# Kernel optimization log

Hardware: AMD Instinct MI355X
Metric: run time of the kernel (lower is better)

The kernel has to match this reference:

```python
import jax, jax.numpy as jnp
import numpy as np
import math

STRIDE = ((2, 2), (4, 4), (8, 8), (16, 16))  # (ws, hs) pairs
D_MODEL = 256
B, H, W = 8, 128, 128
BN_EPS = 1e-5
LEAKY_SLOPE = 0.2


def setup_inputs() -> dict:
    key = jax.random.key(0)
    ks = jax.random.split(key, 8)
    s = 1.0 / math.sqrt(D_MODEL)
    s3 = 1.0 / math.sqrt(D_MODEL * 9)
    return {
        "x": jax.random.normal(ks[0], (B, D_MODEL, H, W), jnp.float32),
        "wq": jax.random.normal(ks[1], (D_MODEL, D_MODEL, 1, 1), jnp.float32) * s,
        "bq": jnp.zeros((D_MODEL,), jnp.float32),
        "wk": jax.random.normal(ks[2], (D_MODEL, D_MODEL, 1, 1), jnp.float32) * s,
        "bk": jnp.zeros((D_MODEL,), jnp.float32),
        "wv": jax.random.normal(ks[3], (D_MODEL, D_MODEL, 1, 1), jnp.float32) * s,
        "bv": jnp.zeros((D_MODEL,), jnp.float32),
        "wo": jax.random.normal(ks[4], (D_MODEL, D_MODEL, 3, 3), jnp.float32) * s3,
        "bo": jnp.zeros((D_MODEL,), jnp.float32),
        "gamma": jnp.ones((D_MODEL,), jnp.float32),
        "beta": jnp.zeros((D_MODEL,), jnp.float32),
    }


def _conv1x1(x, w, bias):
    # 1x1 conv == channel matmul
    return jnp.einsum('bchw,oc->bohw', x, w[:, :, 0, 0]) + bias[None, :, None, None]


def reference(x, wq, bq, wk, bk, wv, bv, wo, bo, gamma, beta):
    b, c, h, w = x.shape
    n = len(STRIDE)
    d_k = c // n
    q = _conv1x1(x, wq, bq)
    k = _conv1x1(x, wk, bk)
    v = _conv1x1(x, wv, bv)
    outs = []
    for idx, (ws, hs) in enumerate(STRIDE):
        lo = idx * d_k
        oh, ow = h // hs, w // ws

        def gather(t):
            # strided patch gather: element (i,j) head <- t[:, :, i::hs, j::ws]
            t = t[:, lo:lo + d_k].reshape(b, d_k, oh, hs, ow, ws)
            return t.transpose(0, 3, 5, 1, 2, 4).reshape(b, hs * ws, d_k * oh * ow)

        qi, ki, vi = gather(q), gather(k), gather(v)
        scale = 1.0 / jnp.sqrt(jnp.asarray(qi.shape[-1], qi.dtype))
        scores = jnp.einsum('bsd,btd->bst', qi, ki) * scale  # [b, hs*ws, hs*ws]
        p = jax.nn.softmax(scores, axis=-1)
        y = jnp.einsum('bst,btd->bsd', p, vi)
        # scatter back exactly as the torch permute(0,3,1,4,2,5): h = i*oh + row
        y = y.reshape(b, hs, ws, d_k, oh, ow).transpose(0, 3, 1, 4, 2, 5).reshape(b, d_k, h, w)
        outs.append(y)
    out = jnp.concatenate(outs, axis=1)  # [b, c, h, w]
    # output_linear: 3x3 conv -> BatchNorm2d (training-mode batch stats) -> LeakyReLU(0.2)
    out = jax.lax.conv_general_dilated(out, wo, (1, 1), 'SAME',
                                       dimension_numbers=('NCHW', 'OIHW', 'NCHW'))
    out = out + bo[None, :, None, None]
    mean = out.mean(axis=(0, 2, 3))
    var = out.var(axis=(0, 2, 3))
    out = (out - mean[None, :, None, None]) * jax.lax.rsqrt(var[None, :, None, None] + BN_EPS)
    out = out * gamma[None, :, None, None] + beta[None, :, None, None]
    return jnp.where(out > 0, out, LEAKY_SLOPE * out)
```

## Files before the change

### kernel.cpp

```cpp
#include <hip/hip_runtime.h>
#include <stdint.h>


#define DEVI static __device__ __forceinline__

typedef short bf8 __attribute__((ext_vector_type(8)));
typedef float f32x4 __attribute__((ext_vector_type(4)));

DEVI unsigned short f2bf(float f) {
  unsigned u = __builtin_bit_cast(unsigned, f);
  u = (u + 0x7fffu + ((u >> 16) & 1u)) >> 16;
  return (unsigned short)u;
}
DEVI float bf2f(unsigned short h) {
  unsigned u = ((unsigned)h) << 16;
  return __builtin_bit_cast(float, u);
}

DEVI void gload16(const void* g, void* l) {
  __builtin_amdgcn_global_load_lds(
      (const __attribute__((address_space(1))) unsigned int*)g,
      (__attribute__((address_space(3))) unsigned int*)l, 16, 0, 0);
}

static const size_t WB_OFF  = 0;
static const size_t WOB_OFF = 393216;
static const size_t QN_OFF  = 1572864;
static const size_t KN_OFF  = QN_OFF + 67108864;
static const size_t VN_OFF  = KN_OFF + 67108864;
static const size_t YN_OFF  = VN_OFF + 67108864;
static const size_t SC_OFF  = YN_OFF + 67108864;
static const size_t PRB_OFF = SC_OFF + 2236928;
static const size_t BNP_OFF = PRB_OFF + 1118464;
static const size_t BNS_OFF = BNP_OFF + 4194304;
static const size_t ZP_OFF  = BNS_OFF + 2048;
static const size_t WS_NEED = ZP_OFF + 256;

__global__ void k_prep(const float* __restrict__ wq, const float* __restrict__ wk,
                       const float* __restrict__ wv, const float* __restrict__ wo,
                       unsigned short* __restrict__ Wb, unsigned short* __restrict__ Wob) {
  int i = blockIdx.x * 256 + threadIdx.x;
  if (i < 196608) {
    int z = i >> 16, r = i & 65535;
    const float* w = (z == 0) ? wq : (z == 1) ? wk : wv;
    Wb[i] = f2bf(w[r]);
  } else {
    int j = i - 196608;
    int o = j / 2304, k = j - o * 2304;
    int e = k >> 8, c = k & 255;
    Wob[j] = f2bf(wo[(o * 256 + c) * 9 + e]);
  }
}

__global__ void k_zero(float* __restrict__ p, int n) {
  int i = blockIdx.x * 256 + threadIdx.x;
  for (; i < n; i += gridDim.x * 256) p[i] = 0.f;
}

__global__ __launch_bounds__(256) void k_qkv(
    const float* __restrict__ x, const unsigned short* __restrict__ Wb,
    const float* __restrict__ bq, const float* __restrict__ bk, const float* __restrict__ bv,
    unsigned short* __restrict__ Qn, unsigned short* __restrict__ Kn,
    unsigned short* __restrict__ Vn) {
  const int pt = blockIdx.x, b = blockIdx.y;
  const int p0 = pt * 64;
  const int tid = threadIdx.x;

  __shared__ __align__(16) unsigned short xt[64 * 256];
  __shared__ __align__(16) unsigned short ot[64 * 256];

  const float* xb = x + (size_t)b * 256 * 16384;
  for (int k = 0; k < 16; ++k) {
    int i = tid + k * 256;
    int c = i >> 4, p4 = (i & 15) * 4;
    float4 v = *(const float4*)(xb + (size_t)c * 16384 + p0 + p4);
    xt[(p4 + 0) * 256 + (c ^ (((p4 + 0) & 7) << 3))] = f2bf(v.x);
    xt[(p4 + 1) * 256 + (c ^ (((p4 + 1) & 7) << 3))] = f2bf(v.y);
    xt[(p4 + 2) * 256 + (c ^ (((p4 + 2) & 7) << 3))] = f2bf(v.z);
    xt[(p4 + 3) * 256 + (c ^ (((p4 + 3) & 7) << 3))] = f2bf(v.w);
  }
  __syncthreads();

  const int wave = tid >> 6, lane = tid & 63;
  const int lr = lane & 15, lk = lane >> 4;
  const int obase = wave * 64;

  for (int z = 0; z < 3; ++z) {
    const unsigned short* Wz = Wb + (size_t)z * 65536;
    f32x4 acc[4][4];
    for (int m = 0; m < 4; ++m)
      for (int n = 0; n < 4; ++n)
        for (int r = 0; r < 4; ++r) acc[m][n][r] = 0.f;

    for (int ks = 0; ks < 8; ++ks) {
      int c0 = ks * 32 + lk * 8;
      bf8 a[4], bb[4];
#pragma unroll
      for (int m = 0; m < 4; ++m)
        a[m] = *(const bf8*)(Wz + (size_t)(obase + m * 16 + lr) * 256 + c0);
#pragma unroll
      for (int n = 0; n < 4; ++n) {
        int p = n * 16 + lr;
        bb[n] = *(const bf8*)(&xt[p * 256 + (c0 ^ ((p & 7) << 3))]);
      }
#pragma unroll
      for (int m = 0; m < 4; ++m)
#pragma unroll
        for (int n = 0; n < 4; ++n)
          acc[m][n] = __builtin_amdgcn_mfma_f32_16x16x32_bf16(a[m], bb[n], acc[m][n], 0, 0, 0);
    }

    const float* bias = (z == 0) ? bq : (z == 1) ? bk : bv;
    unsigned short* On = (z == 0) ? Qn : (z == 1) ? Kn : Vn;
    __syncthreads();
#pragma unroll
    for (int m = 0; m < 4; ++m) {
      int ob4 = obase + m * 16 + lk * 4;
      float4 b4 = *(const float4*)(bias + ob4);
#pragma unroll
      for (int n = 0; n < 4; ++n) {
        int p = n * 16 + lr;
        ushort4 v4;
        v4.x = f2bf(acc[m][n][0] + b4.x);
        v4.y = f2bf(acc[m][n][1] + b4.y);
        v4.z = f2bf(acc[m][n][2] + b4.z);
        v4.w = f2bf(acc[m][n][3] + b4.w);
        *(ushort4*)(&ot[p * 256 + (ob4 ^ ((p & 7) << 3))]) = v4;
      }
    }
    __syncthreads();
    unsigned short* gb = On + ((size_t)b * 16384 + p0) * 256;
#pragma unroll
    for (int i = 0; i < 8; ++i) {
      int ch = tid + i * 256;
      *(uint4*)(gb + ch * 8) = *(const uint4*)(&ot[ch * 8]);
    }
  }
}

template <int IDX>
__global__ __launch_bounds__(256) void k_gram(
    const unsigned short* __restrict__ Qn, const unsigned short* __restrict__ Kn,
    float* __restrict__ scores) {
  constexpr int HS = 2 << IDX, S = HS * HS, OH = 64 >> IDX, NSP = OH * OH;
  constexpr int SPW = (IDX == 2) ? 2 : 8;
  constexpr int DSUB = SPW * 64;
  constexpr int SPB = NSP / 32;
  constexpr int STEPS = SPB / SPW;
  constexpr int ROWS = S;
  constexpr int TPT = S * SPW * 8 / 256;
  constexpr int SCOFF = (IDX == 0) ? 0 : (IDX == 1) ? 128 : 2176;
  constexpr int HC = IDX * 64;
  constexpr int MT = (IDX == 2) ? 4 : 1;

  const int chk = blockIdx.x, b = blockIdx.y;
  const int tid = threadIdx.x;
  const int wave = tid >> 6, lane = tid & 63, lr = lane & 15, lk = lane >> 4;

  __shared__ __align__(16) unsigned short qg[ROWS * DSUB];
  __shared__ __align__(16) unsigned short kg[ROWS * DSUB];
  __shared__ float red[S * S];

  const size_t base = (size_t)b * 16384 * 256;

  f32x4 acc[MT][MT];
  for (int m = 0; m < MT; ++m)
    for (int n = 0; n < MT; ++n)
      for (int r = 0; r < 4; ++r) acc[m][n][r] = 0.f;

  for (int st = 0; st < STEPS; ++st) {
    const int sp0 = chk * SPB + st * SPW;
    __syncthreads();
#pragma unroll
    for (int r = 0; r < TPT; ++r) {
      int task = tid + r * 256;
      int cg = task & 7, pl = task >> 3;
      int spl = pl >> (2 * (IDX + 1)), s = pl & (S - 1);
      int sp = sp0 + spl;
      int ohi = sp >> (6 - IDX), owi = sp & (OH - 1);
      int ii = s >> (IDX + 1), jj = s & (HS - 1);
      int p = (ohi * HS + ii) * 128 + owi * HS + jj;
      size_t gaddr = base + (size_t)p * 256 + HC + ((cg ^ (p & 7)) << 3);
      int laddr = s * DSUB + (((spl * 8 + cg) ^ (s & 7)) << 3);
      *(uint4*)(qg + laddr) = *(const uint4*)(Qn + gaddr);
      *(uint4*)(kg + laddr) = *(const uint4*)(Kn + gaddr);
    }
    __syncthreads();
    if (IDX == 2) {
      int kgid = wave * 4 + lk;
      bf8 a[4], bb[4];
#pragma unroll
      for (int m = 0; m < 4; ++m) {
        int row = m * 16 + lr;
        int off = row * DSUB + ((kgid ^ (row & 7)) << 3);
        a[m] = *(const bf8*)(qg + off);
        bb[m] = *(const bf8*)(kg + off);
      }
#pragma unroll
      for (int m = 0; m < 4; ++m)
#pragma unroll
        for (int n = 0; n < 4; ++n)
          acc[m][n] = __builtin_amdgcn_mfma_f32_16x16x32_bf16(a[m], bb[n], acc[m][n], 0, 0, 0);
    } else {
      int row = lr & (ROWS - 1);
#pragma unroll
      for (int kk = 0; kk < 4; ++kk) {
        int kgid = (wave * 4 + kk) * 4 + lk;
        int off = row * DSUB + ((kgid ^ (row & 7)) << 3);
        bf8 a = *(const bf8*)(qg + off);
        bf8 bb = *(const bf8*)(kg + off);
        acc[0][0] = __builtin_amdgcn_mfma_f32_16x16x32_bf16(a, bb, acc[0][0], 0, 0, 0);
      }
    }
  }

  __syncthreads();
  for (int i2 = tid; i2 < S * S; i2 += 256) red[i2] = 0.f;
  __syncthreads();
  if (IDX == 2) {
#pragma unroll
    for (int m = 0; m < 4; ++m)
#pragma unroll
      for (int n = 0; n < 4; ++n)
#pragma unroll
        for (int r = 0; r < 4; ++r)
          atomicAdd(&red[(m * 16 + lk * 4 + r) * 64 + n * 16 + lr], acc[m][n][r]);
  } else if (IDX == 1) {
#pragma unroll
    for (int r = 0; r < 4; ++r)
      atomicAdd(&red[(lk * 4 + r) * 16 + lr], acc[0][0][r]);
  } else {
    if (lk == 0 && lr < 4) {
#pragma unroll
      for (int r = 0; r < 4; ++r)
        atomicAdd(&red[r * 4 + lr], acc[0][0][r]);
    }
  }
  __syncthreads();
  float* sc = scores + SCOFF + (size_t)b * S * S;
  for (int i2 = tid; i2 < S * S; i2 += 256) atomicAdd(sc + i2, red[i2]);
}

__global__ __launch_bounds__(256) void k_gram3(
    const unsigned short* __restrict__ Qn, const unsigned short* __restrict__ Kn,
    float* __restrict__ part3) {
  const int qc = blockIdx.x, tq = blockIdx.y, b = blockIdx.z;
  const int tid = threadIdx.x;
  const int wave = tid >> 6, lane = tid & 63, lr = lane & 15, lk = lane >> 4;

  __shared__ __align__(16) unsigned short qg[256 * 64];
  __shared__ __align__(16) unsigned short kg[64 * 64];

  const size_t base = (size_t)b * 16384 * 256;

  f32x4 acc[4][4];
  for (int m = 0; m < 4; ++m)
    for (int n = 0; n < 4; ++n)
      for (int r = 0; r < 4; ++r) acc[m][n][r] = 0.f;

  for (int st = 0; st < 8; ++st) {
    int sp = qc * 8 + st;
    int ohi = sp >> 3, owi = sp & 7;
    __syncthreads();
#pragma unroll
    for (int r = 0; r < 8; ++r) {
      int task = tid + r * 256;
      int cg = task & 7, s = task >> 3;
      int p = (ohi * 16 + (s >> 4)) * 128 + owi * 16 + (s & 15);
      uint4 v = *(const uint4*)(Qn + base + (size_t)p * 256 + 192 + ((cg ^ (p & 7)) << 3));
      *(uint4*)(qg + s * 64 + ((cg ^ (s & 7)) << 3)) = v;
    }
#pragma unroll
    for (int r = 0; r < 2; ++r) {
      int task = tid + r * 256;
      int cg = task & 7, tl = task >> 3;
      int p = (ohi * 16 + tq * 4 + (tl >> 4)) * 128 + owi * 16 + (tl & 15);
      uint4 v = *(const uint4*)(Kn + base + (size_t)p * 256 + 192 + ((cg ^ (p & 7)) << 3));
      *(uint4*)(kg + tl * 64 + ((cg ^ (tl & 7)) << 3)) = v;
    }
    __syncthreads();
#pragma unroll
    for (int kk = 0; kk < 2; ++kk) {
      int kgid = kk * 4 + lk;
      bf8 a[4], bb[4];
#pragma unroll
      for (int m = 0; m < 4; ++m) {
        int row = wave * 64 + m * 16 + lr;
        a[m] = *(const bf8*)(qg + row * 64 + ((kgid ^ (row & 7)) << 3));
      }
#pragma unroll
      for (int n = 0; n < 4; ++n) {
        int rowb = n * 16 + lr;
        bb[n] = *(const bf8*)(kg + rowb * 64 + ((kgid ^ (rowb & 7)) << 3));
      }
#pragma unroll
      for (int m = 0; m < 4; ++m)
#pragma unroll
        for (int n = 0; n < 4; ++n)
          acc[m][n] = __builtin_amdgcn_mfma_f32_16x16x32_bf16(a[m], bb[n], acc[m][n], 0, 0, 0);
    }
  }

  float* pb = part3 + (((size_t)qc * 8 + b) * 65536);
#pragma unroll
  for (int m = 0; m < 4; ++m)
#pragma unroll
    for (int r = 0; r < 4; ++r) {
      int srow = wave * 64 + m * 16 + lk * 4 + r;
#pragma unroll
      for (int n = 0; n < 4; ++n)
        pb[srow * 256 + tq * 64 + n * 16 + lr] = acc[m][n][r];
    }
}

__global__ __launch_bounds__(256) void k_softmax(const float* __restrict__ scores,
                                                 unsigned short* __restrict__ prb) {
  const int idx = blockIdx.x, b = blockIdx.y;
  const int S = 4 << (2 * idx);
  const int off = (idx == 0 ? 0 : idx == 1 ? 128 : 2176) + b * S * S;
  const int s = threadIdx.x;
  if (s >= S) return;
  const float scale = rsqrtf(64.0f * (float)(4096 >> (2 * idx)));
  const float* row = scores + off + s * S;
  float m = -1e30f;
  for (int t = 0; t < S; ++t) m = fmaxf(m, row[t]);
  m *= scale;
  float sum = 0.f;
  for (int t = 0; t < S; ++t) sum += __expf(row[t] * scale - m);
  float inv = 1.0f / sum;
  unsigned short* prow = prb + off + s * S;
  for (int t = 0; t < S; ++t) prow[t] = f2bf(__expf(row[t] * scale - m) * inv);
}

__global__ __launch_bounds__(256) void k_softmax3(const float* __restrict__ part3,
                                                  unsigned short* __restrict__ prb) {
  const int sc_ = blockIdx.x, b = blockIdx.y;
  const int tid = threadIdx.x;
  const int s = sc_ * 32 + (tid >> 3);
  const int t0 = (tid & 7) * 32;
  float v[32];
#pragma unroll
  for (int k = 0; k < 32; ++k) v[k] = 0.f;
  for (int q = 0; q < 8; ++q) {
    const float4* pp = (const float4*)(part3 + (((size_t)q * 8 + b) * 256 + s) * 256 + t0);
#pragma unroll
    for (int k = 0; k < 8; ++k) {
      float4 u = pp[k];
      v[k * 4 + 0] += u.x; v[k * 4 + 1] += u.y; v[k * 4 + 2] += u.z; v[k * 4 + 3] += u.w;
    }
  }
  const float scale = 1.0f / 64.0f;
  float m = -1e30f;
#pragma unroll
  for (int k = 0; k < 32; ++k) { v[k] *= scale; m = fmaxf(m, v[k]); }
  m = fmaxf(m, __shfl_xor(m, 1));
  m = fmaxf(m, __shfl_xor(m, 2));
  m = fmaxf(m, __shfl_xor(m, 4));
  float sum = 0.f;
#pragma unroll
  for (int k = 0; k < 32; ++k) { v[k] = __expf(v[k] - m); sum += v[k]; }
  sum += __shfl_xor(sum, 1);
  sum += __shfl_xor(sum, 2);
  sum += __shfl_xor(sum, 4);
  float inv = 1.0f / sum;
  unsigned short* prw = prb + 34944 + (size_t)b * 65536 + s * 256 + t0;
#pragma unroll
  for (int k8 = 0; k8 < 4; ++k8) {
    unsigned short tmp[8];
#pragma unroll
    for (int e = 0; e < 8; ++e) tmp[e] = f2bf(v[k8 * 8 + e] * inv);
    *(uint4*)(prw + k8 * 8) = *(const uint4*)tmp;
  }
}

template <int IDX>
__global__ __launch_bounds__(256) void k_pv(
    const unsigned short* __restrict__ Vn, const unsigned short* __restrict__ prb,
    unsigned short* __restrict__ Yn) {
  constexpr int HS = 2 << IDX, S = HS * HS, OH = 64 >> IDX;
  constexpr int IT = (IDX == 0) ? 8 : (IDX == 1) ? 4 : 1;
  constexpr int POFF = (IDX == 0) ? 0 : (IDX == 1) ? 128 : 2176;
  const int bx = blockIdx.x, b = blockIdx.y;
  const int c = threadIdx.x & 63, spg = threadIdx.x >> 6;
  __shared__ __align__(16) float pl[S * S];
  const unsigned short* pr = prb + POFF + (size_t)b * S * S;
  for (int i = threadIdx.x; i < S * S; i += 256) pl[i] = bf2f(pr[i]);
  __syncthreads();
  const int hc = IDX * 64;
  const unsigned short* vb = Vn + (size_t)b * 16384 * 256;
  unsigned short* yb = Yn + (size_t)b * 16384 * 256;
  for (int it = 0; it < IT; ++it) {
    int sp = bx * (4 * IT) + it * 4 + spg;
    int ohi = sp >> (6 - IDX), owi = sp & (OH - 1);
    float v[S];
#pragma unroll
    for (int t = 0; t < S; ++t) {
      int po = (ohi * HS + t / HS) * 128 + owi * HS + (t % HS);
      v[t] = bf2f(vb[(size_t)po * 256 + ((hc + c) ^ ((po & 7) << 3))]);
    }
    for (int s = 0; s < S; ++s) {
      const float4* p4 = (const float4*)(pl + s * S);
      float a = 0.f;
#pragma unroll
      for (int t4 = 0; t4 < S / 4; ++t4) {
        float4 pp = p4[t4];
        a += pp.x * v[t4 * 4] + pp.y * v[t4 * 4 + 1] + pp.z * v[t4 * 4 + 2] + pp.w * v[t4 * 4 + 3];
      }
      int po = ((s >> (IDX + 1)) * OH + ohi) * 128 + (s & (HS - 1)) * OH + owi;
      yb[(size_t)po * 256 + ((hc + c) ^ ((po & 7) << 3))] = f2bf(a);
    }
  }
}

__global__ __launch_bounds__(256) void k_pv3(
    const unsigned short* __restrict__ Vn, const unsigned short* __restrict__ prb,
    unsigned short* __restrict__ Yn) {
  const int sp = blockIdx.x, b = blockIdx.y;
  const int ohi = sp >> 3, owi = sp & 7;
  const int tid = threadIdx.x;
  __shared__ __align__(16) unsigned short vl[64 * 256];
  const unsigned short* vb = Vn + (size_t)b * 16384 * 256;
  {
    int t = tid;
    int po = (ohi * 16 + (t >> 4)) * 128 + owi * 16 + (t & 15);
    const unsigned short* src = vb + (size_t)po * 256;
    int xv = (po & 7) << 3;
#pragma unroll
    for (int g = 0; g < 8; ++g) {
      ushort4 lo = *(const ushort4*)(src + ((192 + g * 8) ^ xv));
      ushort4 hi = *(const ushort4*)(src + ((192 + g * 8) ^ xv) + 4);
      unsigned short vv[8] = {lo.x, lo.y, lo.z, lo.w, hi.x, hi.y, hi.z, hi.w};
#pragma unroll
      for (int e = 0; e < 8; ++e) {
        int cc = g * 8 + e;
        vl[cc * 256 + (t ^ ((cc & 7) << 3))] = vv[e];
      }
    }
  }
  __syncthreads();

  const int wave = tid >> 6, lane = tid & 63;
  const int lr = lane & 15, lk = lane >> 4;
  const int sb = wave * 64;
  const unsigned short* pr = prb + 34944 + (size_t)b * 65536;

  f32x4 acc[4][4];
  for (int m = 0; m < 4; ++m)
    for (int n = 0; n < 4; ++n)
      for (int r = 0; r < 4; ++r) acc[m][n][r] = 0.f;

  for (int kk = 0; kk < 8; ++kk) {
    int t0 = kk * 32 + lk * 8;
    bf8 a[4], bb[4];
#pragma unroll
    for (int m = 0; m < 4; ++m)
      a[m] = *(const bf8*)(pr + (size_t)(sb + m * 16 + lr) * 256 + t0);
#pragma unroll
    for (int n = 0; n < 4; ++n) {
      int cc = n * 16 + lr;
      bb[n] = *(const bf8*)(&vl[cc * 256 + (t0 ^ ((cc & 7) << 3))]);
    }
#pragma unroll
    for (int m = 0; m < 4; ++m)
#pragma unroll
      for (int n = 0; n < 4; ++n)
        acc[m][n] = __builtin_amdgcn_mfma_f32_16x16x32_bf16(a[m], bb[n], acc[m][n], 0, 0, 0);
  }

  unsigned short* yb = Yn + (size_t)b * 16384 * 256;
#pragma unroll
  for (int m = 0; m < 4; ++m) {
#pragma unroll
    for (int r = 0; r < 4; ++r) {
      int s = sb + m * 16 + lk * 4 + r;
      int si = s >> 4, sj = s & 15;
      int po = (si * 8 + ohi) * 128 + sj * 8 + owi;
#pragma unroll
      for (int n = 0; n < 4; ++n) {
        int cc = 192 + n * 16 + lr;
        yb[(size_t)po * 256 + (cc ^ (owi << 3))] = f2bf(acc[m][n][r]);
      }
    }
  }
}

__global__ __launch_bounds__(512, 2) void k_conv(
    const unsigned short* __restrict__ Yn, const unsigned short* __restrict__ Wob,
    const float* __restrict__ bo, const unsigned short* __restrict__ zp,
    float* __restrict__ out, float* __restrict__ bnp) {
  __shared__ __align__(16) unsigned short lds[8][8192];

  const int bid = blockIdx.x;
  const int swz = (bid & 7) * 64 + (bid >> 3);
  const int b = swz >> 6, tile = swz & 63;
  const int y0 = (tile >> 3) * 16, x0 = (tile & 7) * 16;
  const int tid = threadIdx.x;
  const int wave = tid >> 6, lane = tid & 63;
  const int lr = lane & 15, lk = lane >> 4;
  const int wm = wave >> 2, wn = wave & 3;
  const int cg = lane & 7;

  const unsigned short* yb = Yn + (size_t)b * 16384 * 256;

  auto STAGE = [&](int slot, int w, int KT) {
    if (w < 2) {
      const unsigned short* wsrc = Wob + (KT >> 2) * 256 + (KT & 3) * 64;
#pragma unroll
      for (int j = 0; j < 2; ++j) {
        int rp = (wave * 2 + j) * 8 + (lane >> 3);
        int o = ((rp >> 6) & 1) * 128 + w * 64 + (rp & 63);
        int kg = cg ^ (rp & 7);
        gload16(wsrc + o * 2304 + (kg << 3), &lds[slot][(wave * 2 + j) * 512]);
      }
    } else {
      int e = KT >> 2;
      int dy = e / 3 - 1, dx = e % 3 - 1, c8 = (KT & 3) * 8;
#pragma unroll
      for (int j = 0; j < 2; ++j) {
        int rp = (wave * 2 + j) * 8 + (lane >> 3);
        int n = ((rp >> 5) & 3) * 64 + (w - 2) * 32 + (rp & 31);
        int kg = cg ^ (rp & 7);
        int h = y0 + (n >> 4) + dy, ww = x0 + (n & 15) + dx;
        const unsigned short* src = zp;
        if (h >= 0 && h < 128 && ww >= 0 && ww < 128) {
          int pp = h * 128 + ww;
          src = yb + (size_t)pp * 256 + ((c8 + (kg ^ (pp & 7))) << 3);
        }
        gload16(src, &lds[slot][(wave * 2 + j) * 512]);
      }
    }
  };

  f32x4 acc[8][4];
#pragma unroll
  for (int m = 0; m < 8; ++m)
#pragma unroll
    for (int n = 0; n < 4; ++n)
#pragma unroll
      for (int r = 0; r < 4; ++r) acc[m][n][r] = 0.f;

  STAGE(0, 0, 0); STAGE(1, 1, 0); STAGE(2, 2, 0); STAGE(3, 3, 0); STAGE(4, 0, 1);

  for (int gg = 0; gg < 18; ++gg) {
#pragma unroll
    for (int sub = 0; sub < 8; ++sub) {
      const int g = sub >> 2;
      const int r = sub & 3;
      const int P = gg * 8 + sub;
      if (P <= 138) {
        STAGE((sub + 5) & 7, (sub + 5) & 3, gg * 2 + ((sub + 5) >> 2));
        asm volatile("s_waitcnt vmcnt(6)" ::: "memory");
      } else if (P == 140) {
        asm volatile("s_waitcnt vmcnt(0)" ::: "memory");
      }
      __builtin_amdgcn_s_barrier();
      asm volatile("" ::: "memory");
      const int mh = r >> 1, nh = r & 1;
      const int sA = g * 4 + mh, sB = g * 4 + 2 + nh;
      bf8 a[4][2], bq2[2][2];
#pragma unroll
      for (int m2 = 0; m2 < 4; ++m2) {
        int row = wm * 64 + m2 * 16 + lr;
#pragma unroll
        for (int kk = 0; kk < 2; ++kk)
          a[m2][kk] = *(const bf8*)(&lds[sA][row * 64 + (((kk * 4 + lk) ^ (row & 7)) << 3)]);
      }
#pragma unroll
      for (int n2 = 0; n2 < 2; ++n2) {
        int row = wn * 32 + n2 * 16 + lr;
#pragma unroll
        for (int kk = 0; kk < 2; ++kk)
          bq2[n2][kk] = *(const bf8*)(&lds[sB][row * 64 + (((kk * 4 + lk) ^ (row & 7)) << 3)]);
      }
      __builtin_amdgcn_s_setprio(1);
#pragma unroll
      for (int kk = 0; kk < 2; ++kk)
#pragma unroll
        for (int m2 = 0; m2 < 4; ++m2)
#pragma unroll
          for (int n2 = 0; n2 < 2; ++n2)
            acc[mh * 4 + m2][nh * 2 + n2] = __builtin_amdgcn_mfma_f32_16x16x32_bf16(
                a[m2][kk], bq2[n2][kk], acc[mh * 4 + m2][nh * 2 + n2], 0, 0, 0);
      __builtin_amdgcn_s_setprio(0);
      asm volatile("" ::: "memory");
      __builtin_amdgcn_s_barrier();
    }
  }

  __syncthreads();
  float* ob = out + (size_t)b * 256 * 16384;
  float* red1 = (float*)&lds[0][0];
  float* red2 = red1 + 1024;
#pragma unroll
  for (int m = 0; m < 8; ++m) {
#pragma unroll
    for (int r = 0; r < 4; ++r) {
      int o = wm * 128 + m * 16 + lk * 4 + r;
      float bvv = bo[o];
      float s1 = 0.f, s2 = 0.f;
#pragma unroll
      for (int n = 0; n < 4; ++n) {
        int pix = wn * 64 + n * 16 + lr;
        int py = pix >> 4, px = pix & 15;
        float v = acc[m][n][r] + bvv;
        ob[(size_t)o * 16384 + (y0 + py) * 128 + x0 + px] = v;
        s1 += v;
        s2 += v * v;
      }
      for (int off = 1; off < 16; off <<= 1) {
        s1 += __shfl_xor(s1, off, 64);
        s2 += __shfl_xor(s2, off, 64);
      }
      if (lr == 0) {
        int ol = m * 16 + lk * 4 + r;
        red1[wave * 128 + ol] = s1;
        red2[wave * 128 + ol] = s2;
      }
    }
  }
  __syncthreads();
  {
    int o = tid & 255, stat = tid >> 8;
    int wm2 = o >> 7, ol = o & 127;
    const float* rd = stat ? red2 : red1;
    float s = rd[(wm2 * 4 + 0) * 128 + ol] + rd[(wm2 * 4 + 1) * 128 + ol] +
              rd[(wm2 * 4 + 2) * 128 + ol] + rd[(wm2 * 4 + 3) * 128 + ol];
    bnp[((size_t)(b * 64 + tile) * 256 + o) * 2 + stat] = s;
  }
}

__global__ __launch_bounds__(256) void k_bnred(
    const float* __restrict__ bnp, const float* __restrict__ gamma,
    const float* __restrict__ beta, float* __restrict__ bns) {
  const int o = blockIdx.x;
  const int tid = threadIdx.x;
  float s1 = 0.f, s2 = 0.f;
  for (int k = tid; k < 512; k += 256) {
    s1 += bnp[((size_t)k * 256 + o) * 2 + 0];
    s2 += bnp[((size_t)k * 256 + o) * 2 + 1];
  }
  __shared__ float r1[256], r2[256];
  r1[tid] = s1; r2[tid] = s2;
  __syncthreads();
  for (int off = 128; off > 0; off >>= 1) {
    if (tid < off) { r1[tid] += r1[tid + off]; r2[tid] += r2[tid + off]; }
    __syncthreads();
  }
  if (tid == 0) {
    const float cnt = 8.0f * 16384.0f;
    float mean = r1[0] / cnt;
    float var = r2[0] / cnt - mean * mean;
    float sc = gamma[o] * rsqrtf(var + 1e-5f);
    bns[o] = sc;
    bns[256 + o] = beta[o] - mean * sc;
  }
}

__global__ void k_bnapply(float* __restrict__ out, const float* __restrict__ bns) {
  size_t i = ((size_t)blockIdx.x * 256 + threadIdx.x) * 4;
  const size_t total = 33554432;
  const size_t stride = (size_t)gridDim.x * 256 * 4;
  for (; i < total; i += stride) {
    float4 v = *(float4*)(out + i);
    int o = (int)((i >> 14) & 255);
    float sc = bns[o], shv = bns[256 + o];
    v.x = v.x * sc + shv; v.x = v.x > 0.f ? v.x : 0.2f * v.x;
    v.y = v.y * sc + shv; v.y = v.y > 0.f ? v.y : 0.2f * v.y;
    v.z = v.z * sc + shv; v.z = v.z > 0.f ? v.z : 0.2f * v.z;
    v.w = v.w * sc + shv; v.w = v.w > 0.f ? v.w : 0.2f * v.w;
    *(float4*)(out + i) = v;
  }
}

extern "C" void kernel_launch(void* const* d_in, const int* in_sizes, int n_in,
                              void* d_out, int out_size, void* d_ws, size_t ws_size,
                              hipStream_t stream) {
  if (ws_size < WS_NEED) return;

  const float* x     = (const float*)d_in[0];
  const float* wq    = (const float*)d_in[1];
  const float* bq    = (const float*)d_in[2];
  const float* wk    = (const float*)d_in[3];
  const float* bk    = (const float*)d_in[4];
  const float* wv    = (const float*)d_in[5];
  const float* bv    = (const float*)d_in[6];
  const float* wo    = (const float*)d_in[7];
  const float* bo    = (const float*)d_in[8];
  const float* gamma = (const float*)d_in[9];
  const float* beta  = (const float*)d_in[10];
  float* out = (float*)d_out;
  char* ws = (char*)d_ws;

  unsigned short* Wb  = (unsigned short*)(ws + WB_OFF);
  unsigned short* Wob = (unsigned short*)(ws + WOB_OFF);
  unsigned short* Qn  = (unsigned short*)(ws + QN_OFF);
  unsigned short* Kn  = (unsigned short*)(ws + KN_OFF);
  unsigned short* Vn  = (unsigned short*)(ws + VN_OFF);
  unsigned short* Yn  = (unsigned short*)(ws + YN_OFF);
  float* part3 = (float*)(ws + YN_OFF);
  float* scores = (float*)(ws + SC_OFF);
  unsigned short* prb = (unsigned short*)(ws + PRB_OFF);
  float* bnp    = (float*)(ws + BNP_OFF);
  float* bns    = (float*)(ws + BNS_OFF);
  unsigned short* zp = (unsigned short*)(ws + ZP_OFF);

  k_prep<<<dim3(3072), dim3(256), 0, stream>>>(wq, wk, wv, wo, Wb, Wob);
  k_zero<<<dim3(137), dim3(256), 0, stream>>>(scores, 34944);
  k_zero<<<dim3(1), dim3(64), 0, stream>>>((float*)zp, 64);
  k_qkv<<<dim3(256, 8), dim3(256), 0, stream>>>(x, Wb, bq, bk, bv, Qn, Kn, Vn);
  k_gram<0><<<dim3(32, 8), dim3(256), 0, stream>>>(Qn, Kn, scores);
  k_gram<1><<<dim3(32, 8), dim3(256), 0, stream>>>(Qn, Kn, scores);
  k_gram<2><<<dim3(32, 8), dim3(256), 0, stream>>>(Qn, Kn, scores);
  k_gram3<<<dim3(8, 4, 8), dim3(256), 0, stream>>>(Qn, Kn, part3);
  k_softmax<<<dim3(3, 8), dim3(256), 0, stream>>>(scores, prb);
  k_softmax3<<<dim3(8, 8), dim3(256), 0, stream>>>(part3, prb);
  k_pv<0><<<dim3(128, 8), dim3(256), 0, stream>>>(Vn, prb, Yn);
  k_pv<1><<<dim3(64, 8), dim3(256), 0, stream>>>(Vn, prb, Yn);
  k_pv<2><<<dim3(64, 8), dim3(256), 0, stream>>>(Vn, prb, Yn);
  k_pv3<<<dim3(64, 8), dim3(256), 0, stream>>>(Vn, prb, Yn);
  k_conv<<<dim3(512), dim3(512), 0, stream>>>(Yn, Wob, bo, zp, out, bnp);
  k_bnred<<<dim3(256), dim3(256), 0, stream>>>(bnp, gamma, beta, bns);
  k_bnapply<<<dim3(4096), dim3(256), 0, stream>>>(out, bns);
}
```

Before: 591.7 us.

## Restructure conv pipeline with A-fragment reuse and bf16 intermediate output

The conv main loop is rewritten as macro-unrolled phases: the stage order is reordered so A fragments loaded from LDS are reused across two consecutive phases, and the trailing barrier per phase is dropped. The pre-BN conv result is now written as bf16 to workspace rather than fp32 to the output, and the BN apply kernel reads bf16 and writes fp32. This cuts LDS reads and global traffic for the intermediate. It adds bf16 rounding error before normalization, and removing a barrier risks LDS slot overwrite races.

```diff
diff --git a/kernel.cpp b/kernel.cpp
--- a/kernel.cpp
+++ b/kernel.cpp
@@ -484,10 +484,52 @@
   }
 }
 
+#define CONV_PHASE(KT_, R_, PK_, DOSTAGE_, WAITMODE_)                            \
+  do {                                                                           \
+    if (DOSTAGE_) {                                                              \
+      constexpr int type_ = (R_ == 0) ? 0 : (R_ == 1) ? 2 : (R_ == 2) ? 3 : 1;   \
+      STAGE((1 - (PK_)) * 4 + (R_), type_, (KT_) + 1);                           \
+    }                                                                            \
+    if ((WAITMODE_) == 0) { asm volatile("s_waitcnt vmcnt(6)" ::: "memory"); }   \
+    else if ((WAITMODE_) == 1) { asm volatile("s_waitcnt vmcnt(0)" ::: "memory"); } \
+    __builtin_amdgcn_s_barrier();                                                \
+    asm volatile("" ::: "memory");                                               \
+    {                                                                            \
+      constexpr int mh_ = (R_) >> 1, nh_ = (R_) & 1;                             \
+      constexpr int sA_ = (PK_) * 4 + (mh_ ? 3 : 0);                             \
+      constexpr int sB_ = (PK_) * 4 + (nh_ ? 2 : 1);                             \
+      if (nh_ == 0) {                                                            \
+        _Pragma("unroll") for (int m2 = 0; m2 < 4; ++m2) {                       \
+          int row = wm * 64 + m2 * 16 + lr;                                      \
+          _Pragma("unroll") for (int kk = 0; kk < 2; ++kk)                       \
+            areg[m2][kk] = *(const bf8*)(&lds[sA_][row * 64 +                    \
+                (((kk * 4 + lk) ^ (row & 7)) << 3)]);                            \
+        }                                                                        \
+      }                                                                          \
+      bf8 breg[2][2];                                                            \
+      _Pragma("unroll") for (int n2 = 0; n2 < 2; ++n2) {                         \
+        int row = wn * 32 + n2 * 16 + lr;                                        \
+        _Pragma("unroll") for (int kk = 0; kk < 2; ++kk)                         \
+          breg[n2][kk] = *(const bf8*)(&lds[sB_][row * 64 +                      \
+              (((kk * 4 + lk) ^ (row & 7)) << 3)]);                              \
+      }                                                                          \
+      __builtin_amdgcn_s_setprio(1);                                             \
+      _Pragma("unroll") for (int kk = 0; kk < 2; ++kk)                           \
+        _Pragma("unroll") for (int m2 = 0; m2 < 4; ++m2)                         \
+          _Pragma("unroll") for (int n2 = 0; n2 < 2; ++n2)                       \
+            acc[mh_ * 4 + m2][nh_ * 2 + n2] =                                    \
+                __builtin_amdgcn_mfma_f32_16x16x32_bf16(                         \
+                    areg[m2][kk], breg[n2][kk],                                  \
+                    acc[mh_ * 4 + m2][nh_ * 2 + n2], 0, 0, 0);                   \
+      __builtin_amdgcn_s_setprio(0);                                             \
+      asm volatile("" ::: "memory");                                             \
+    }                                                                            \
+  } while (0)
+
 __global__ __launch_bounds__(512, 2) void k_conv(
     const unsigned short* __restrict__ Yn, const unsigned short* __restrict__ Wob,
     const float* __restrict__ bo, const unsigned short* __restrict__ zp,
-    float* __restrict__ out, float* __restrict__ bnp) {
+    unsigned short* __restrict__ co, float* __restrict__ bnp) {
   __shared__ __align__(16) unsigned short lds[8][8192];
 
   const int bid = blockIdx.x;
@@ -502,13 +544,13 @@
 
   const unsigned short* yb = Yn + (size_t)b * 16384 * 256;
 
-  auto STAGE = [&](int slot, int w, int KT) {
-    if (w < 2) {
+  auto STAGE = [&](int slot, int type, int KT) {
+    if (type < 2) {
       const unsigned short* wsrc = Wob + (KT >> 2) * 256 + (KT & 3) * 64;
 #pragma unroll
       for (int j = 0; j < 2; ++j) {
         int rp = (wave * 2 + j) * 8 + (lane >> 3);
-        int o = ((rp >> 6) & 1) * 128 + w * 64 + (rp & 63);
+        int o = ((rp >> 6) & 1) * 128 + type * 64 + (rp & 63);
         int kg = cg ^ (rp & 7);
         gload16(wsrc + o * 2304 + (kg << 3), &lds[slot][(wave * 2 + j) * 512]);
       }
@@ -518,7 +560,7 @@
 #pragma unroll
       for (int j = 0; j < 2; ++j) {
         int rp = (wave * 2 + j) * 8 + (lane >> 3);
-        int n = ((rp >> 5) & 3) * 64 + (w - 2) * 32 + (rp & 31);
+        int n = ((rp >> 5) & 3) * 64 + (type - 2) * 32 + (rp & 31);
         int kg = cg ^ (rp & 7);
         int h = y0 + (n >> 4) + dy, ww = x0 + (n & 15) + dx;
         const unsigned short* src = zp;
@@ -539,56 +581,33 @@
 #pragma unroll
       for (int r = 0; r < 4; ++r) acc[m][n][r] = 0.f;
 
-  STAGE(0, 0, 0); STAGE(1, 1, 0); STAGE(2, 2, 0); STAGE(3, 3, 0); STAGE(4, 0, 1);
-
-  for (int gg = 0; gg < 18; ++gg) {
-#pragma unroll
-    for (int sub = 0; sub < 8; ++sub) {
-      const int g = sub >> 2;
-      const int r = sub & 3;
-      const int P = gg * 8 + sub;
-      if (P <= 138) {
-        STAGE((sub + 5) & 7, (sub + 5) & 3, gg * 2 + ((sub + 5) >> 2));
-        asm volatile("s_waitcnt vmcnt(6)" ::: "memory");
-      } else if (P == 140) {
-        asm volatile("s_waitcnt vmcnt(0)" ::: "memory");
-      }
-      __builtin_amdgcn_s_barrier();
-      asm volatile("" ::: "memory");
-      const int mh = r >> 1, nh = r & 1;
-      const int sA = g * 4 + mh, sB = g * 4 + 2 + nh;
-      bf8 a[4][2], bq2[2][2];
-#pragma unroll
-      for (int m2 = 0; m2 < 4; ++m2) {
-        int row = wm * 64 + m2 * 16 + lr;
-#pragma unroll
-        for (int kk = 0; kk < 2; ++kk)
-          a[m2][kk] = *(const bf8*)(&lds[sA][row * 64 + (((kk * 4 + lk) ^ (row & 7)) << 3)]);
-      }
-#pragma unroll
-      for (int n2 = 0; n2 < 2; ++n2) {
-        int row = wn * 32 + n2 * 16 + lr;
-#pragma unroll
-        for (int kk = 0; kk < 2; ++kk)
-          bq2[n2][kk] = *(const bf8*)(&lds[sB][row * 64 + (((kk * 4 + lk) ^ (row & 7)) << 3)]);
-      }
-      __builtin_amdgcn_s_setprio(1);
-#pragma unroll
-      for (int kk = 0; kk < 2; ++kk)
-#pragma unroll
-        for (int m2 = 0; m2 < 4; ++m2)
-#pragma unroll
-          for (int n2 = 0; n2 < 2; ++n2)
-            acc[mh * 4 + m2][nh * 2 + n2] = __builtin_amdgcn_mfma_f32_16x16x32_bf16(
-                a[m2][kk], bq2[n2][kk], acc[mh * 4 + m2][nh * 2 + n2], 0, 0, 0);
-      __builtin_amdgcn_s_setprio(0);
-      asm volatile("" ::: "memory");
-      __builtin_amdgcn_s_barrier();
-    }
-  }
-
-  __syncthreads();
-  float* ob = out + (size_t)b * 256 * 16384;
+  bf8 areg[4][2];
+
+  STAGE(0, 0, 0); STAGE(1, 2, 0); STAGE(2, 3, 0); STAGE(3, 1, 0);
+  asm volatile("s_waitcnt vmcnt(0)" ::: "memory");
+
+  for (int gg = 0; gg < 17; ++gg) {
+    const int k0 = gg * 2;
+    CONV_PHASE(k0, 0, 0, true, 0);
+    CONV_PHASE(k0, 1, 0, true, 0);
+    CONV_PHASE(k0, 2, 0, true, 0);
+    CONV_PHASE(k0, 3, 0, true, 0);
+    CONV_PHASE(k0 + 1, 0, 1, true, 0);
+    CONV_PHASE(k0 + 1, 1, 1, true, 0);
+    CONV_PHASE(k0 + 1, 2, 1, true, 0);
+    CONV_PHASE(k0 + 1, 3, 1, true, 0);
+  }
+  CONV_PHASE(34, 0, 0, true, 0);
+  CONV_PHASE(34, 1, 0, true, 0);
+  CONV_PHASE(34, 2, 0, true, 0);
+  CONV_PHASE(34, 3, 0, true, 0);
+  CONV_PHASE(35, 0, 1, false, 1);
+  CONV_PHASE(35, 1, 1, false, 2);
+  CONV_PHASE(35, 2, 1, false, 2);
+  CONV_PHASE(35, 3, 1, false, 2);
+
+  __syncthreads();
+  unsigned short* cb = co + (size_t)b * 256 * 16384;
   float* red1 = (float*)&lds[0][0];
   float* red2 = red1 + 1024;
 #pragma unroll
@@ -603,7 +622,7 @@
         int pix = wn * 64 + n * 16 + lr;
         int py = pix >> 4, px = pix & 15;
         float v = acc[m][n][r] + bvv;
-        ob[(size_t)o * 16384 + (y0 + py) * 128 + x0 + px] = v;
+        cb[(size_t)o * 16384 + (y0 + py) * 128 + x0 + px] = f2bf(v);
         s1 += v;
         s2 += v * v;
       }
@@ -656,19 +675,24 @@
   }
 }
 
-__global__ void k_bnapply(float* __restrict__ out, const float* __restrict__ bns) {
-  size_t i = ((size_t)blockIdx.x * 256 + threadIdx.x) * 4;
+__global__ void k_bnapply(const unsigned short* __restrict__ co, float* __restrict__ out,
+                          const float* __restrict__ bns) {
+  size_t i = ((size_t)blockIdx.x * 256 + threadIdx.x) * 8;
   const size_t total = 33554432;
-  const size_t stride = (size_t)gridDim.x * 256 * 4;
+  const size_t stride = (size_t)gridDim.x * 256 * 8;
   for (; i < total; i += stride) {
-    float4 v = *(float4*)(out + i);
+    uint4 v = *(const uint4*)(co + i);
     int o = (int)((i >> 14) & 255);
     float sc = bns[o], shv = bns[256 + o];
-    v.x = v.x * sc + shv; v.x = v.x > 0.f ? v.x : 0.2f * v.x;
-    v.y = v.y * sc + shv; v.y = v.y > 0.f ? v.y : 0.2f * v.y;
-    v.z = v.z * sc + shv; v.z = v.z > 0.f ? v.z : 0.2f * v.z;
-    v.w = v.w * sc + shv; v.w = v.w > 0.f ? v.w : 0.2f * v.w;
-    *(float4*)(out + i) = v;
+    const unsigned short* pv = (const unsigned short*)&v;
+    float r[8];
+#pragma unroll
+    for (int e = 0; e < 8; ++e) {
+      float f = bf2f(pv[e]) * sc + shv;
+      r[e] = f > 0.f ? f : 0.2f * f;
+    }
+    *(float4*)(out + i) = *(const float4*)&r[0];
+    *(float4*)(out + i + 4) = *(const float4*)&r[4];
   }
 }
 
@@ -698,6 +722,7 @@
   unsigned short* Vn  = (unsigned short*)(ws + VN_OFF);
   unsigned short* Yn  = (unsigned short*)(ws + YN_OFF);
   float* part3 = (float*)(ws + YN_OFF);
+  unsigned short* co = (unsigned short*)(ws + QN_OFF);
   float* scores = (float*)(ws + SC_OFF);
   unsigned short* prb = (unsigned short*)(ws + PRB_OFF);
   float* bnp    = (float*)(ws + BNP_OFF);
@@ -718,7 +743,7 @@
   k_pv<1><<<dim3(64, 8), dim3(256), 0, stream>>>(Vn, prb, Yn);
   k_pv<2><<<dim3(64, 8), dim3(256), 0, stream>>>(Vn, prb, Yn);
   k_pv3<<<dim3(64, 8), dim3(256), 0, stream>>>(Vn, prb, Yn);
-  k_conv<<<dim3(512), dim3(512), 0, stream>>>(Yn, Wob, bo, zp, out, bnp);
+  k_conv<<<dim3(512), dim3(512), 0, stream>>>(Yn, Wob, bo, zp, co, bnp);
   k_bnred<<<dim3(256), dim3(256), 0, stream>>>(bnp, gamma, beta, bns);
-  k_bnapply<<<dim3(4096), dim3(256), 0, stream>>>(out, bns);
-}
+  k_bnapply<<<dim3(4096), dim3(256), 0, stream>>>(co, out, bns);
+}
```

Result: faster. 571.1 us (-3.5%).
